# Kernel tuning notes

Measured on AMD Instinct MI355X. Metric: run time of the kernel, lower is better.

Reference implementation:

```python
import jax, jax.numpy as jnp
import numpy as np

B, D_IN, EMB = 8192, 4000, 96
H0, H1 = 2048, 1024
NB, NC, OPT = 8, 8, 32
NE = NB * NC  # 64 experts (total contests)


def setup_inputs() -> dict:
    key = jax.random.key(0)
    ks = jax.random.split(key, 10)
    scale = lambda fan_in: jnp.sqrt(2.0 / fan_in)  # kaiming_normal-ish
    return {
        "inputs": jax.random.normal(ks[0], (B, D_IN), dtype=jnp.float32),
        "emb_table": jax.random.normal(ks[1], (NE, EMB), dtype=jnp.float32) * scale(EMB),
        "W0": jax.random.normal(ks[2], (D_IN + EMB, H0), dtype=jnp.float32) * scale(D_IN + EMB),
        "b0": jnp.zeros((H0,), dtype=jnp.float32),
        "W1": jax.random.normal(ks[3], (H0, H1), dtype=jnp.float32) * scale(H0),
        "b1": jnp.zeros((H1,), dtype=jnp.float32),
        "We": jax.random.normal(ks[4], (NE, H1, OPT), dtype=jnp.float32) * scale(H1),
        "be": jnp.zeros((NE, OPT), dtype=jnp.float32),
        "ballot_number": jax.random.randint(ks[5], (B,), 0, NB, dtype=jnp.int32),
        "contest_number": jax.random.randint(ks[6], (B,), 0, NC, dtype=jnp.int32),
        "batches": B,
    }


def reference(inputs, emb_table, W0, b0, W1, b1, We, be,
              ballot_number, contest_number, batches):
    # flat expert index per sample: index_of[ballot][contest] with equal-size ballots
    expert = ballot_number * NC + contest_number                  # [B]
    x = inputs.reshape(batches, -1)                               # [B, D_IN]
    emb = emb_table[expert]                                       # [B, EMB] (gather)
    h = jnp.concatenate([emb, x], axis=1)                         # [B, D_IN+EMB]
    h = jax.nn.relu(h @ W0 + b0)                                  # fc0 (dropout = id at eval)
    h = jax.nn.relu(h @ W1 + b1)                                  # fc1
    # per-sample routed linear: gather expert weights, batched matvec
    out = jnp.einsum("bd,bdo->bo", h, We[expert]) + be[expert]    # [B, OPT]
    return jax.nn.sigmoid(out)
```

## Files before the change

kernel.cpp:

```cpp
#include <hip/hip_runtime.h>
#include <math.h>

typedef __attribute__((ext_vector_type(8))) short short8;
typedef __attribute__((ext_vector_type(4))) float f32x4;

#define B_SZ 8192
#define D_INN 4000
#define EMBD 96
#define H0D 2048
#define H1D 1024
#define KDIM 4096

#define MFMA_BF16 __builtin_amdgcn_mfma_f32_16x16x32_bf16

__device__ __forceinline__ unsigned short f2bf(float f) {
  union { float f; unsigned u; } v; v.f = f;
  unsigned r = v.u + 0x7FFFu + ((v.u >> 16) & 1u);
  return (unsigned short)(r >> 16);
}
__device__ __forceinline__ float bf2f(unsigned short h) {
  union { unsigned u; float f; } v; v.u = ((unsigned)h) << 16;
  return v.f;
}
__device__ __forceinline__ void gld_lds16(const void* g, void* l) {
  __builtin_amdgcn_global_load_lds(
      (const __attribute__((address_space(1))) unsigned int*)g,
      (__attribute__((address_space(3))) unsigned int*)l, 16, 0, 0);
}

__global__ __launch_bounds__(256) void transpose_cvt(
    const float* __restrict__ in, unsigned short* __restrict__ out, int R, int C) {
  __shared__ float tile[32][33];
  int c0 = blockIdx.x * 32, r0 = blockIdx.y * 32;
  int tc = threadIdx.x & 31, tr = threadIdx.x >> 5;
#pragma unroll
  for (int i = 0; i < 4; ++i) {
    int r = tr + i * 8;
    tile[r][tc] = in[(size_t)(r0 + r) * C + (c0 + tc)];
  }
  __syncthreads();
#pragma unroll
  for (int i = 0; i < 4; ++i) {
    int rr = tr + i * 8;
    out[(size_t)(c0 + rr) * R + (r0 + tc)] = f2bf(tile[tc][rr]);
  }
}

__global__ __launch_bounds__(256) void transpose_cvt_we(
    const float* __restrict__ in, unsigned short* __restrict__ out) {
  __shared__ float tile[32][33];
  const int e = blockIdx.y, r0 = blockIdx.x * 32;
  const float* src = in + (size_t)e * 32768;
  unsigned short* dst = out + (size_t)e * 32768;
  int tc = threadIdx.x & 31, tr = threadIdx.x >> 5;
#pragma unroll
  for (int i = 0; i < 4; ++i) {
    int r = tr + i * 8;
    tile[r][tc] = src[(size_t)(r0 + r) * 32 + tc];
  }
  __syncthreads();
#pragma unroll
  for (int i = 0; i < 4; ++i) {
    int rr = tr + i * 8;
    dst[(size_t)rr * H1D + r0 + tc] = f2bf(tile[tc][rr]);
  }
}

__global__ __launch_bounds__(256) void build_A(
    const float* __restrict__ inputs, const float* __restrict__ emb,
    const int* __restrict__ ballot, const int* __restrict__ contest,
    unsigned short* __restrict__ A) {
  int gid = blockIdx.x * 256 + threadIdx.x;
  int b = gid >> 9, c = gid & 511;
  const float* src;
  if (c < EMBD / 8) {
    int e = ballot[b] * 8 + contest[b];
    src = emb + (size_t)e * EMBD + c * 8;
  } else {
    src = inputs + (size_t)b * D_INN + (c - EMBD / 8) * 8;
  }
  float4 v0 = *(const float4*)src;
  float4 v1 = *(const float4*)(src + 4);
  unsigned short r[8];
  r[0] = f2bf(v0.x); r[1] = f2bf(v0.y); r[2] = f2bf(v0.z); r[3] = f2bf(v0.w);
  r[4] = f2bf(v1.x); r[5] = f2bf(v1.y); r[6] = f2bf(v1.z); r[7] = f2bf(v1.w);
  *reinterpret_cast<short8*>(A + (size_t)b * KDIM + c * 8) =
      *reinterpret_cast<const short8*>(r);
}

template <int K>
__global__ __launch_bounds__(1024) void gemm_nt_16w(
    const unsigned short* __restrict__ A, const unsigned short* __restrict__ Bt,
    const float* __restrict__ bias, unsigned short* __restrict__ C,
    int N, int NBN) {
  constexpr int SLOT = 16384;
  __shared__ char lds[6 * SLOT];

  const int tid = threadIdx.x;
  const int w = tid >> 6, l = tid & 63;
  const int lr = l & 15, kg = l >> 4;
  const int wm = w >> 2, wn = w & 3;

  int swz = (blockIdx.x & 7) * ((int)gridDim.x >> 3) + ((int)blockIdx.x >> 3);
  const int bm = swz / NBN, bn = swz - bm * NBN;
  const int NT = K >> 5;

  const int srow = tid >> 2;
  const int swzsl = (tid & 3) ^ ((srow >> 1) & 3);
  const unsigned short* gaB = A + (size_t)(bm * 256 + srow) * K + swzsl * 8;
  const unsigned short* gbB = Bt + (size_t)(bn * 256 + srow) * K + swzsl * 8;

  const int xo = (kg ^ ((lr >> 1) & 3)) << 4;
  const int aoff = (wm * 64 + lr) * 64 + xo;
  const int boff = (wn * 64 + lr) * 64 + xo;

  f32x4 acc[4][4] = {};

  auto stageA = [&](int t, int rbuf) {
    gld_lds16(gaB + t * 32, lds + rbuf * SLOT + tid * 16);
  };
  auto stageB = [&](int t, int rbuf) {
    gld_lds16(gbB + t * 32, lds + 3 * SLOT + rbuf * SLOT + tid * 16);
  };

  stageA(0, 0); stageB(0, 0);
  stageA(1, 1); stageB(1, 1);
  asm volatile("s_waitcnt vmcnt(2)" ::: "memory");
  __builtin_amdgcn_s_barrier();

  int rb = 0;
  for (int t = 0; t < NT; ++t) {
    int rb2 = rb + 2; if (rb2 >= 3) rb2 -= 3;
    const char* pa = lds + rb * SLOT + aoff;
    const char* pb = lds + 3 * SLOT + rb * SLOT + boff;

    short8 a0[2], bfr[4];
#pragma unroll
    for (int mi = 0; mi < 2; ++mi) a0[mi] = *(const short8*)(pa + mi * 1024);
#pragma unroll
    for (int ni = 0; ni < 4; ++ni) bfr[ni] = *(const short8*)(pb + ni * 1024);
    if (t + 2 < NT) stageA(t + 2, rb2);
    __builtin_amdgcn_s_setprio(1);
#pragma unroll
    for (int mi = 0; mi < 2; ++mi)
#pragma unroll
      for (int ni = 0; ni < 4; ++ni)
        acc[mi][ni] = MFMA_BF16(a0[mi], bfr[ni], acc[mi][ni], 0, 0, 0);
    __builtin_amdgcn_s_setprio(0);

    short8 a1[2];
#pragma unroll
    for (int mi = 0; mi < 2; ++mi) a1[mi] = *(const short8*)(pa + (2 + mi) * 1024);
    if (t + 2 < NT) stageB(t + 2, rb2);
    __builtin_amdgcn_s_setprio(1);
#pragma unroll
    for (int mi = 0; mi < 2; ++mi)
#pragma unroll
      for (int ni = 0; ni < 4; ++ni)
        acc[2 + mi][ni] = MFMA_BF16(a1[mi], bfr[ni], acc[2 + mi][ni], 0, 0, 0);
    __builtin_amdgcn_s_setprio(0);

    if (t + 2 < NT) {
      asm volatile("s_waitcnt vmcnt(2)" ::: "memory");
      __builtin_amdgcn_s_barrier();
    } else if (t + 1 < NT) {
      asm volatile("s_waitcnt vmcnt(0)" ::: "memory");
      __builtin_amdgcn_s_barrier();
    }
    rb = rb + 1; if (rb >= 3) rb = 0;
  }

#pragma unroll
  for (int mi = 0; mi < 4; ++mi) {
    const int row0 = bm * 256 + wm * 64 + mi * 16 + kg * 4;
#pragma unroll
    for (int ni = 0; ni < 4; ++ni) {
      const int col = bn * 256 + wn * 64 + ni * 16 + lr;
      const float bv = bias[col];
#pragma unroll
      for (int j = 0; j < 4; ++j) {
        float v = acc[mi][ni][j] + bv;
        v = v > 0.f ? v : 0.f;
        C[(size_t)(row0 + j) * N + col] = f2bf(v);
      }
    }
  }
}

__global__ __launch_bounds__(1024) void gemm2_16w(
    const unsigned short* __restrict__ A, const unsigned short* __restrict__ Bt,
    const float* __restrict__ bias, unsigned short* __restrict__ C) {
  constexpr int K = H0D, N = H1D, NBN = 4;
  constexpr int ASLOT = 16384, BSLOT = 32768;
  constexpr int NT = K / 64;
  __shared__ char lds[3 * ASLOT + 3 * BSLOT];

  const int tid = threadIdx.x;
  const int w = tid >> 6, l = tid & 63;
  const int lr = l & 15, kg = l >> 4;
  const int wm = w >> 2, wn = w & 3;

  int swz = (blockIdx.x & 7) * ((int)gridDim.x >> 3) + ((int)blockIdx.x >> 3);
  const int bm = swz / NBN, bn = swz - bm * NBN;

  const int srow = tid >> 3;
  const int sslot = (tid & 7) ^ (srow & 7);
  const unsigned short* gaB = A + (size_t)(bm * 128 + srow) * K + sslot * 8;
  const unsigned short* gb0 = Bt + (size_t)(bn * 256 + srow) * K + sslot * 8;
  const unsigned short* gb1 = gb0 + (size_t)128 * K;

  f32x4 acc[2][4] = {};

  auto stage = [&](int t, int rbuf) {
    gld_lds16(gaB + t * 64, lds + rbuf * ASLOT + tid * 16);
    char* lb = lds + 3 * ASLOT + rbuf * BSLOT + tid * 16;
    gld_lds16(gb0 + t * 64, lb);
    gld_lds16(gb1 + t * 64, lb + 16384);
  };

  auto rdrow = [&](const char* base, int row, int ks) -> short8 {
    return *(const short8*)(base + row * 128 + (((ks << 2) | kg) ^ (row & 7)) * 16);
  };

  stage(0, 0);
  stage(1, 1);
  asm volatile("s_waitcnt vmcnt(3)" ::: "memory");
  __builtin_amdgcn_s_barrier();

  int rb = 0;
  for (int t = 0; t < NT; ++t) {
    int rb2 = rb + 2; if (rb2 >= 3) rb2 -= 3;
    const char* pa = lds + rb * ASLOT;
    const char* pb = lds + 3 * ASLOT + rb * BSLOT;

    short8 a[2][2], b[4][2];
#pragma unroll
    for (int mi = 0; mi < 2; ++mi)
#pragma unroll
      for (int ks = 0; ks < 2; ++ks)
        a[mi][ks] = rdrow(pa, wm * 32 + mi * 16 + lr, ks);
#pragma unroll
    for (int ni = 0; ni < 4; ++ni)
#pragma unroll
      for (int ks = 0; ks < 2; ++ks)
        b[ni][ks] = rdrow(pb, wn * 64 + ni * 16 + lr, ks);
    if (t + 2 < NT) stage(t + 2, rb2);
    __builtin_amdgcn_s_setprio(1);
#pragma unroll
    for (int mi = 0; mi < 2; ++mi)
#pragma unroll
      for (int ni = 0; ni < 4; ++ni)
#pragma unroll
        for (int ks = 0; ks < 2; ++ks)
          acc[mi][ni] = MFMA_BF16(a[mi][ks], b[ni][ks], acc[mi][ni], 0, 0, 0);
    __builtin_amdgcn_s_setprio(0);

    if (t + 2 < NT) {
      asm volatile("s_waitcnt vmcnt(3)" ::: "memory");
      __builtin_amdgcn_s_barrier();
    } else if (t + 1 < NT) {
      asm volatile("s_waitcnt vmcnt(0)" ::: "memory");
      __builtin_amdgcn_s_barrier();
    }
    rb = rb + 1; if (rb >= 3) rb = 0;
  }

#pragma unroll
  for (int mi = 0; mi < 2; ++mi) {
    const int row0 = bm * 128 + wm * 32 + mi * 16 + kg * 4;
#pragma unroll
    for (int ni = 0; ni < 4; ++ni) {
      const int col = bn * 256 + wn * 64 + ni * 16 + lr;
      const float bv = bias[col];
#pragma unroll
      for (int j = 0; j < 4; ++j) {
        float v = acc[mi][ni][j] + bv;
        v = v > 0.f ? v : 0.f;
        C[(size_t)(row0 + j) * N + col] = f2bf(v);
      }
    }
  }
}

__global__ __launch_bounds__(256) void expert_head_mfma(
    const unsigned short* __restrict__ h1, const unsigned short* __restrict__ Wet,
    const float* __restrict__ be, const int* __restrict__ ballot,
    const int* __restrict__ contest, float* __restrict__ out) {
  const int e = blockIdx.x;
  __shared__ unsigned short sidx[1024];
  __shared__ int scnt;
  if (threadIdx.x == 0) scnt = 0;
  __syncthreads();
  for (int i = threadIdx.x; i < B_SZ; i += 256)
    if (ballot[i] * 8 + contest[i] == e) {
      int p = atomicAdd(&scnt, 1);
      if (p < 1024) sidx[p] = (unsigned short)i;
    }
  __syncthreads();
  const int cnt = min(scnt, 1024);
  const int w = threadIdx.x >> 6, l = threadIdx.x & 63;
  const int lr = l & 15, kg = l >> 4;
  const unsigned short* wbase = Wet + (size_t)e * 32768;
  for (int c0 = w * 32; c0 < cnt; c0 += 128) {
    const int ns = min(32, cnt - c0);
    f32x4 acc[2][2] = {};
    int ridx[2];
#pragma unroll
    for (int mi = 0; mi < 2; ++mi) {
      int rr = mi * 16 + lr;
      ridx[mi] = sidx[c0 + (rr < ns ? rr : 0)];
    }
#pragma unroll 4
    for (int kk = 0; kk < 32; ++kk) {
      short8 a0 = *(const short8*)(h1 + (size_t)ridx[0] * H1D + kk * 32 + kg * 8);
      short8 a1 = *(const short8*)(h1 + (size_t)ridx[1] * H1D + kk * 32 + kg * 8);
      short8 b0 = *(const short8*)(wbase + (size_t)lr * H1D + kk * 32 + kg * 8);
      short8 b1 = *(const short8*)(wbase + (size_t)(16 + lr) * H1D + kk * 32 + kg * 8);
      acc[0][0] = MFMA_BF16(a0, b0, acc[0][0], 0, 0, 0);
      acc[0][1] = MFMA_BF16(a0, b1, acc[0][1], 0, 0, 0);
      acc[1][0] = MFMA_BF16(a1, b0, acc[1][0], 0, 0, 0);
      acc[1][1] = MFMA_BF16(a1, b1, acc[1][1], 0, 0, 0);
    }
#pragma unroll
    for (int mi = 0; mi < 2; ++mi)
#pragma unroll
      for (int ni = 0; ni < 2; ++ni)
#pragma unroll
        for (int j = 0; j < 4; ++j) {
          int row = mi * 16 + kg * 4 + j;
          int col = ni * 16 + lr;
          if (row < ns) {
            float x = acc[mi][ni][j] + be[e * 32 + col];
            out[(size_t)sidx[c0 + row] * 32 + col] = 1.f / (1.f + expf(-x));
          }
        }
  }
}

extern "C" void kernel_launch(void* const* d_in, const int* in_sizes, int n_in,
                              void* d_out, int out_size, void* d_ws, size_t ws_size,
                              hipStream_t stream) {
  const float* inputs = (const float*)d_in[0];
  const float* emb    = (const float*)d_in[1];
  const float* W0     = (const float*)d_in[2];
  const float* b0     = (const float*)d_in[3];
  const float* W1     = (const float*)d_in[4];
  const float* b1     = (const float*)d_in[5];
  const float* We     = (const float*)d_in[6];
  const float* be     = (const float*)d_in[7];
  const int* ballot   = (const int*)d_in[8];
  const int* contest  = (const int*)d_in[9];
  float* out = (float*)d_out;

  char* ws = (char*)d_ws;
  unsigned short* A   = (unsigned short*)(ws);
  unsigned short* W0t = (unsigned short*)(ws + 67108864);
  unsigned short* h0  = (unsigned short*)(ws + 83886080);
  unsigned short* W1t = (unsigned short*)(ws + 117440512);
  unsigned short* h1  = (unsigned short*)(ws + 121634816);
  unsigned short* Wet = (unsigned short*)(ws);

  dim3 blk(256);
  transpose_cvt<<<dim3(H0D / 32, KDIM / 32, 1), blk, 0, stream>>>(W0, W0t, KDIM, H0D);
  transpose_cvt<<<dim3(H1D / 32, H0D / 32, 1), blk, 0, stream>>>(W1, W1t, H0D, H1D);
  build_A<<<dim3(B_SZ * 512 / 256), blk, 0, stream>>>(inputs, emb, ballot, contest, A);
  gemm_nt_16w<KDIM><<<dim3(256), dim3(1024), 0, stream>>>(A, W0t, b0, h0, H0D, H0D / 256);
  transpose_cvt_we<<<dim3(32, 64), blk, 0, stream>>>(We, Wet);
  gemm2_16w<<<dim3(256), dim3(1024), 0, stream>>>(h0, W1t, b1, h1);
  expert_head_mfma<<<dim3(64), blk, 0, stream>>>(h1, Wet, be, ballot, contest, out);
}
```

Measured before the change: 235.7 us.

## Merge weight transposes, retile second GEMM to 8 waves, split expert head blocks

After: 220.4 us. 6.5% less time.

```diff
diff --git a/kernel.cpp b/kernel.cpp
--- a/kernel.cpp
+++ b/kernel.cpp
@@ -28,10 +28,20 @@
       (__attribute__((address_space(3))) unsigned int*)l, 16, 0, 0);
 }
 
-__global__ __launch_bounds__(256) void transpose_cvt(
-    const float* __restrict__ in, unsigned short* __restrict__ out, int R, int C) {
+__global__ __launch_bounds__(256) void transpose_w01(
+    const float* __restrict__ W0, const float* __restrict__ W1,
+    unsigned short* __restrict__ W0t, unsigned short* __restrict__ W1t) {
   __shared__ float tile[32][33];
-  int c0 = blockIdx.x * 32, r0 = blockIdx.y * 32;
+  const int bid = blockIdx.x;
+  const float* in; unsigned short* out; int R, C, c0, r0;
+  if (bid < 8192) {
+    in = W0; out = W0t; R = KDIM; C = H0D;
+    c0 = (bid & 63) * 32; r0 = (bid >> 6) * 32;
+  } else {
+    int x = bid - 8192;
+    in = W1; out = W1t; R = H0D; C = H1D;
+    c0 = (x & 31) * 32; r0 = (x >> 5) * 32;
+  }
   int tc = threadIdx.x & 31, tr = threadIdx.x >> 5;
 #pragma unroll
   for (int i = 0; i < 4; ++i) {
@@ -187,13 +197,13 @@
   }
 }
 
-__global__ __launch_bounds__(1024) void gemm2_16w(
+__global__ __launch_bounds__(512) void gemm2_8w(
     const unsigned short* __restrict__ A, const unsigned short* __restrict__ Bt,
     const float* __restrict__ bias, unsigned short* __restrict__ C) {
   constexpr int K = H0D, N = H1D, NBN = 4;
-  constexpr int ASLOT = 16384, BSLOT = 32768;
-  constexpr int NT = K / 64;
-  __shared__ char lds[3 * ASLOT + 3 * BSLOT];
+  constexpr int ASLOT = 8192, BSLOT = 16384;
+  constexpr int NT = K >> 5;
+  __shared__ char lds[3 * (ASLOT + BSLOT)];
 
   const int tid = threadIdx.x;
   const int w = tid >> 6, l = tid & 63;
@@ -203,23 +213,23 @@
   int swz = (blockIdx.x & 7) * ((int)gridDim.x >> 3) + ((int)blockIdx.x >> 3);
   const int bm = swz / NBN, bn = swz - bm * NBN;
 
-  const int srow = tid >> 3;
-  const int sslot = (tid & 7) ^ (srow & 7);
-  const unsigned short* gaB = A + (size_t)(bm * 128 + srow) * K + sslot * 8;
-  const unsigned short* gb0 = Bt + (size_t)(bn * 256 + srow) * K + sslot * 8;
+  const int srow = tid >> 2;
+  const int swzsl = (tid & 3) ^ ((srow >> 1) & 3);
+  const unsigned short* gaB = A + (size_t)(bm * 128 + srow) * K + swzsl * 8;
+  const unsigned short* gb0 = Bt + (size_t)(bn * 256 + srow) * K + swzsl * 8;
   const unsigned short* gb1 = gb0 + (size_t)128 * K;
 
-  f32x4 acc[2][4] = {};
+  const int xo = (kg ^ ((lr >> 1) & 3)) << 4;
+  const int aoff = (wm * 64 + lr) * 64 + xo;
+  const int boff = (wn * 64 + lr) * 64 + xo;
+
+  f32x4 acc[4][4] = {};
 
   auto stage = [&](int t, int rbuf) {
-    gld_lds16(gaB + t * 64, lds + rbuf * ASLOT + tid * 16);
+    gld_lds16(gaB + t * 32, lds + rbuf * ASLOT + tid * 16);
     char* lb = lds + 3 * ASLOT + rbuf * BSLOT + tid * 16;
-    gld_lds16(gb0 + t * 64, lb);
-    gld_lds16(gb1 + t * 64, lb + 16384);
-  };
-
-  auto rdrow = [&](const char* base, int row, int ks) -> short8 {
-    return *(const short8*)(base + row * 128 + (((ks << 2) | kg) ^ (row & 7)) * 16);
+    gld_lds16(gb0 + t * 32, lb);
+    gld_lds16(gb1 + t * 32, lb + 8192);
   };
 
   stage(0, 0);
@@ -230,29 +240,21 @@
   int rb = 0;
   for (int t = 0; t < NT; ++t) {
     int rb2 = rb + 2; if (rb2 >= 3) rb2 -= 3;
-    const char* pa = lds + rb * ASLOT;
-    const char* pb = lds + 3 * ASLOT + rb * BSLOT;
-
-    short8 a[2][2], b[4][2];
-#pragma unroll
-    for (int mi = 0; mi < 2; ++mi)
-#pragma unroll
-      for (int ks = 0; ks < 2; ++ks)
-        a[mi][ks] = rdrow(pa, wm * 32 + mi * 16 + lr, ks);
-#pragma unroll
-    for (int ni = 0; ni < 4; ++ni)
-#pragma unroll
-      for (int ks = 0; ks < 2; ++ks)
-        b[ni][ks] = rdrow(pb, wn * 64 + ni * 16 + lr, ks);
+    const char* pa = lds + rb * ASLOT + aoff;
+    const char* pb = lds + 3 * ASLOT + rb * BSLOT + boff;
+
+    short8 a[4], b[4];
+#pragma unroll
+    for (int mi = 0; mi < 4; ++mi) a[mi] = *(const short8*)(pa + mi * 1024);
+#pragma unroll
+    for (int ni = 0; ni < 4; ++ni) b[ni] = *(const short8*)(pb + ni * 1024);
     if (t + 2 < NT) stage(t + 2, rb2);
     __builtin_amdgcn_s_setprio(1);
 #pragma unroll
-    for (int mi = 0; mi < 2; ++mi)
+    for (int mi = 0; mi < 4; ++mi)
 #pragma unroll
       for (int ni = 0; ni < 4; ++ni)
-#pragma unroll
-        for (int ks = 0; ks < 2; ++ks)
-          acc[mi][ni] = MFMA_BF16(a[mi][ks], b[ni][ks], acc[mi][ni], 0, 0, 0);
+        acc[mi][ni] = MFMA_BF16(a[mi], b[ni], acc[mi][ni], 0, 0, 0);
     __builtin_amdgcn_s_setprio(0);
 
     if (t + 2 < NT) {
@@ -266,8 +268,8 @@
   }
 
 #pragma unroll
-  for (int mi = 0; mi < 2; ++mi) {
-    const int row0 = bm * 128 + wm * 32 + mi * 16 + kg * 4;
+  for (int mi = 0; mi < 4; ++mi) {
+    const int row0 = bm * 128 + wm * 64 + mi * 16 + kg * 4;
 #pragma unroll
     for (int ni = 0; ni < 4; ++ni) {
       const int col = bn * 256 + wn * 64 + ni * 16 + lr;
@@ -286,12 +288,13 @@
     const unsigned short* __restrict__ h1, const unsigned short* __restrict__ Wet,
     const float* __restrict__ be, const int* __restrict__ ballot,
     const int* __restrict__ contest, float* __restrict__ out) {
-  const int e = blockIdx.x;
+  const int e = blockIdx.x >> 1, half = blockIdx.x & 1;
   __shared__ unsigned short sidx[1024];
   __shared__ int scnt;
   if (threadIdx.x == 0) scnt = 0;
   __syncthreads();
-  for (int i = threadIdx.x; i < B_SZ; i += 256)
+  const int lo = half * (B_SZ / 2), hi = lo + B_SZ / 2;
+  for (int i = lo + threadIdx.x; i < hi; i += 256)
     if (ballot[i] * 8 + contest[i] == e) {
       int p = atomicAdd(&scnt, 1);
       if (p < 1024) sidx[p] = (unsigned short)i;
@@ -361,11 +364,10 @@
   unsigned short* Wet = (unsigned short*)(ws);
 
   dim3 blk(256);
-  transpose_cvt<<<dim3(H0D / 32, KDIM / 32, 1), blk, 0, stream>>>(W0, W0t, KDIM, H0D);
-  transpose_cvt<<<dim3(H1D / 32, H0D / 32, 1), blk, 0, stream>>>(W1, W1t, H0D, H1D);
+  transpose_w01<<<dim3(10240), blk, 0, stream>>>(W0, W1, W0t, W1t);
   build_A<<<dim3(B_SZ * 512 / 256), blk, 0, stream>>>(inputs, emb, ballot, contest, A);
   gemm_nt_16w<KDIM><<<dim3(256), dim3(1024), 0, stream>>>(A, W0t, b0, h0, H0D, H0D / 256);
   transpose_cvt_we<<<dim3(32, 64), blk, 0, stream>>>(We, Wet);
-  gemm2_16w<<<dim3(256), dim3(1024), 0, stream>>>(h0, W1t, b1, h1);
-  expert_head_mfma<<<dim3(64), blk, 0, stream>>>(h1, Wet, be, ballot, contest, out);
-}
+  gemm2_8w<<<dim3(256), dim3(512), 0, stream>>>(h0, W1t, b1, h1);
+  expert_head_mfma<<<dim3(128), blk, 0, stream>>>(h1, Wet, be, ballot, contest, out);
+}
```
